# Performance work log

Hardware: AMD Instinct MI355X
Metric: run time of the kernel (lower is better)

The kernel has to match this reference:

```python
import jax, jax.numpy as jnp
import numpy as np

B = 1
DIM = 2048
N_HEADS = 16
HEAD_DIM = 128
RANK = 128
ALPHA = 128.0
L_NOISE = 2048
L_COND = 1024
N_LORAS = 1
EPS = 1e-6
NEG = -1e20


def setup_inputs() -> dict:
    key = jax.random.key(0)
    ks = jax.random.split(key, 24)
    inp = {}
    inp["noise_flat"] = jax.random.normal(ks[0], (B, L_NOISE, DIM), jnp.float32)
    inp["cond_flat"] = jax.random.normal(ks[1], (B, L_COND, DIM), jnp.float32)
    # RoPE freqs in TE 'bshd' convention: (L, head_dim), halves duplicated
    inv_freq = 1.0 / (10000.0 ** (jnp.arange(0, HEAD_DIM, 2, dtype=jnp.float32) / HEAD_DIM))
    pos = jnp.arange(L_NOISE + L_COND, dtype=jnp.float32)
    fr = pos[:, None] * inv_freq[None, :]
    fr = jnp.concatenate([fr, fr], axis=-1)  # (L, HEAD_DIM)
    inp["noise_rope"] = fr[:L_NOISE]
    inp["cond_rope"] = fr[L_NOISE:]
    std = 0.02
    inp["Wq"] = jax.random.normal(ks[2], (DIM, DIM), jnp.float32) * std
    inp["Wk"] = jax.random.normal(ks[3], (DIM, DIM), jnp.float32) * std
    inp["Wv"] = jax.random.normal(ks[4], (DIM, DIM), jnp.float32) * std
    inp["Wo"] = jax.random.normal(ks[5], (DIM, DIM), jnp.float32) * std
    inp["bq"] = jnp.zeros((DIM,), jnp.float32)
    inp["bk"] = jnp.zeros((DIM,), jnp.float32)
    inp["bv"] = jnp.zeros((DIM,), jnp.float32)
    inp["bo"] = jnp.zeros((DIM,), jnp.float32)
    inp["q_norm_scale"] = jnp.ones((HEAD_DIM,), jnp.float32)
    inp["k_norm_scale"] = jnp.ones((HEAD_DIM,), jnp.float32)
    inp["v_norm_scale"] = jnp.ones((HEAD_DIM,), jnp.float32)
    # LoRA: down ~ N(0, 1/rank); up small nonzero (torch inits zeros, made nonzero for a meaningful baseline)
    for name, ki in zip(["q", "k", "v", "o"], range(6, 10)):
        k1, k2 = jax.random.split(ks[ki])
        inp[f"lora_{name}_down"] = jax.random.normal(k1, (DIM, RANK), jnp.float32) / RANK
        inp[f"lora_{name}_up"] = jax.random.normal(k2, (RANK, DIM), jnp.float32) * 0.01
    return inp


def _rms_norm(x, scale):
    return x * jax.lax.rsqrt(jnp.mean(x * x, axis=-1, keepdims=True) + EPS) * scale


def _rotate_half(x):
    x1, x2 = jnp.split(x, 2, axis=-1)
    return jnp.concatenate([-x2, x1], axis=-1)


def _apply_rope(x, freqs):
    # x: (B, L, H, D), freqs: (L, D)
    cos = jnp.cos(freqs)[None, :, None, :]
    sin = jnp.sin(freqs)[None, :, None, :]
    return x * cos + _rotate_half(x) * sin


def _block_mask():
    # noise rows attend to everything; cond block i attends only to itself
    L = L_NOISE + L_COND * N_LORAS
    idx = jnp.arange(L)
    is_noise = idx < L_NOISE
    blk = (idx - L_NOISE) // L_COND
    allowed = is_noise[:, None] | (
        (~is_noise[:, None]) & (~is_noise[None, :]) & (blk[:, None] == blk[None, :])
    )
    return jnp.where(allowed, 0.0, NEG).astype(jnp.float32)  # (L, L)


def _cond_mask(i, L):
    idx = jnp.arange(L)
    start = L_NOISE + i * L_COND
    return ((idx >= start) & (idx < start + L_COND)).astype(jnp.float32)[None, :, None]


def reference(noise_flat, cond_flat, noise_rope, cond_rope,
              Wq, Wk, Wv, Wo, bq, bk, bv, bo,
              q_norm_scale, k_norm_scale, v_norm_scale,
              lora_q_down, lora_q_up, lora_k_down, lora_k_up,
              lora_v_down, lora_v_up, lora_o_down, lora_o_up):
    joint = jnp.concatenate([noise_flat, cond_flat], axis=1)  # (B, L, D)
    rope = jnp.concatenate([noise_rope, cond_rope], axis=0)   # (L, HEAD_DIM)
    L = joint.shape[1]
    scale_lora = ALPHA / RANK
    m = _cond_mask(0, L)  # n_loras = 1, lora_weight = 1.0
    jm = joint * m

    def lora(x_masked, Wd, Wu):
        return (x_masked @ Wd) @ Wu * scale_lora

    q = joint @ Wq + bq + lora(jm, lora_q_down, lora_q_up)
    k = joint @ Wk + bk + lora(jm, lora_k_down, lora_k_up)
    v = joint @ Wv + bv + lora(jm, lora_v_down, lora_v_up)

    q = q.reshape(B, L, N_HEADS, HEAD_DIM)
    k = k.reshape(B, L, N_HEADS, HEAD_DIM)
    v = v.reshape(B, L, N_HEADS, HEAD_DIM)
    q = _rms_norm(q, q_norm_scale)
    k = _rms_norm(k, k_norm_scale)
    v = _rms_norm(v, v_norm_scale)
    q = _apply_rope(q, rope)
    k = _apply_rope(k, rope)

    bias = _block_mask()[None, None]  # (1,1,L,L)
    scores = jnp.einsum('bqhd,bkhd->bhqk', q, k) / jnp.sqrt(jnp.float32(HEAD_DIM)) + bias
    attn = jax.nn.softmax(scores, axis=-1)
    x = jnp.einsum('bhqk,bkhd->bqhd', attn, v).reshape(B, L, DIM)

    out = x @ Wo + bo + lora(x * m, lora_o_down, lora_o_up)
    return out[:, :L_NOISE, :], out[:, L_NOISE:, :]
```

## Files before the change

kernel.cpp:

```cpp
#include <hip/hip_runtime.h>

typedef _Float16 f16;
typedef _Float16 half8 __attribute__((ext_vector_type(8)));
typedef float floatx4 __attribute__((ext_vector_type(4)));

#define L_TOT   3072
#define L_NZ    2048
#define DIM_C   2048
#define NH      16
#define HD      128

__device__ __forceinline__ void gl_lds16(const f16* g, f16* l) {
    __builtin_amdgcn_global_load_lds((__attribute__((address_space(1))) void*)g,
                                     (__attribute__((address_space(3))) void*)l,
                                     16, 0, 0);
}

__global__ void sentinel_kernel(float* out) { out[0] = 1.0e6f; }

__global__ __launch_bounds__(256)
void cast_joint(const float* __restrict__ noise, const float* __restrict__ cond,
                f16* __restrict__ out) {
    int i = (blockIdx.x * 256 + threadIdx.x) * 4;
    const float* src; int off;
    if (i < 2048 * 2048) { src = noise; off = i; }
    else                 { src = cond;  off = i - 2048 * 2048; }
    float4 v = *(const float4*)(src + off);
    out[i+0] = (f16)v.x; out[i+1] = (f16)v.y;
    out[i+2] = (f16)v.z; out[i+3] = (f16)v.w;
}

__global__ __launch_bounds__(256)
void transpose_cast4(const float* __restrict__ s0, const float* __restrict__ s1,
                     const float* __restrict__ s2, const float* __restrict__ s3,
                     f16* __restrict__ dstBase, int R, int C, long long outBatch) {
    const float* in = (blockIdx.z == 0) ? s0 : (blockIdx.z == 1) ? s1 : (blockIdx.z == 2) ? s2 : s3;
    f16* out = dstBase + (long long)blockIdx.z * outBatch;
    __shared__ f16 tile[32][33];
    int x = threadIdx.x & 31, y0 = threadIdx.x >> 5;
    int r0 = blockIdx.y * 32, c0 = blockIdx.x * 32;
#pragma unroll
    for (int i = 0; i < 4; ++i) {
        int y = y0 + i * 8;
        tile[y][x] = (f16)in[(size_t)(r0 + y) * C + (c0 + x)];
    }
    __syncthreads();
#pragma unroll
    for (int i = 0; i < 4; ++i) {
        int y = y0 + i * 8;
        out[(size_t)(c0 + y) * R + (r0 + x)] = tile[x][y];
    }
}

template<int WRITE_HALF, int ACCUM, int ADD_BIAS, int MODE>
__global__ __launch_bounds__(256, 2)
void gemm_tn(const f16* __restrict__ A, const f16* __restrict__ BT,
             void* __restrict__ Cv,
             const float* __restrict__ bias0, const float* __restrict__ bias1,
             const float* __restrict__ bias2,
             int M, int N, int K, int lda, int ldb, int ldc, float cscale) {
    __shared__ __align__(16) f16 lds[2][2][128 * 64];
    const int tid  = threadIdx.x;
    const int lane = tid & 63, wave = tid >> 6;
    const int m0 = blockIdx.y * 128, n0 = blockIdx.x * 128;
    const int wr = wave >> 1, wc = wave & 1;
    floatx4 acc[4][4] = {};

    if (MODE == 2) A += (size_t)(n0 >> 11) * 128;

    const int r0i = tid >> 3;
    const int gch = (tid & 7) ^ (r0i & 7);
    const f16* gA0 = A  + (size_t)(m0 + r0i) * lda + gch * 8;
    const f16* gB0 = BT + (size_t)(n0 + r0i) * ldb + gch * 8;
    const int ldsW = wave * 512;

    auto stage = [&](int buf, int k0) {
#pragma unroll
        for (int is = 0; is < 4; ++is)
            gl_lds16(gA0 + k0 + (size_t)is * 32 * lda, &lds[buf][0][0] + is * 2048 + ldsW);
#pragma unroll
        for (int is = 0; is < 4; ++is)
            gl_lds16(gB0 + k0 + (size_t)is * 32 * ldb, &lds[buf][1][0] + is * 2048 + ldsW);
    };

    const int rl = lane & 15, cq = lane >> 4;

    const int nIter = K >> 6;
    stage(0, 0);
    int cur = 0;
    for (int t = 0; t < nIter; ++t) {
        const int k0n = (t + 1 < nIter) ? (t + 1) * 64 : 0;
        stage(cur ^ 1, k0n);
        asm volatile("s_waitcnt vmcnt(8)" ::: "memory");
        __builtin_amdgcn_s_barrier();
        __builtin_amdgcn_sched_barrier(0);

#pragma unroll
        for (int kh = 0; kh < 2; ++kh) {
            half8 af[4], bf[4];
#pragma unroll
            for (int m = 0; m < 4; ++m) {
                int row = wr * 64 + m * 16 + rl;
                int pos = (kh * 4 + cq) ^ (row & 7);
                af[m] = *(const half8*)(&lds[cur][0][row * 64 + pos * 8]);
            }
#pragma unroll
            for (int n = 0; n < 4; ++n) {
                int row = wc * 64 + n * 16 + rl;
                int pos = (kh * 4 + cq) ^ (row & 7);
                bf[n] = *(const half8*)(&lds[cur][1][row * 64 + pos * 8]);
            }
#pragma unroll
            for (int m = 0; m < 4; ++m)
#pragma unroll
                for (int n = 0; n < 4; ++n)
                    acc[m][n] = __builtin_amdgcn_mfma_f32_16x16x32_f16(af[m], bf[n], acc[m][n], 0, 0, 0);
        }
        __builtin_amdgcn_s_barrier();
        __builtin_amdgcn_sched_barrier(0);
        cur ^= 1;
    }

    const int rq = lane >> 4;
    const float* bias = bias0;
    size_t cbase = 0;
    if (MODE == 1 || MODE == 2) {
        int chunk = n0 >> 11;
        if (MODE == 1) bias = (chunk == 0) ? bias0 : ((chunk == 1) ? bias1 : bias2);
        cbase = (size_t)chunk * ((size_t)L_TOT * DIM_C);
    }
#pragma unroll
    for (int m = 0; m < 4; ++m) {
        int row = m0 + wr * 64 + m * 16 + rq * 4;
#pragma unroll
        for (int n = 0; n < 4; ++n) {
            int col = n0 + wc * 64 + n * 16 + rl;
            int ccol = (MODE == 1 || MODE == 2) ? (col & 2047) : col;
            float badd = ADD_BIAS ? bias[ccol] : 0.0f;
#pragma unroll
            for (int j = 0; j < 4; ++j) {
                float v = acc[m][n][j] * cscale + badd;
                size_t idx = cbase + (size_t)(row + j) * ldc + ccol;
                if (WRITE_HALF) {
                    f16* C = (f16*)Cv;
                    if (ACCUM) v += (float)C[idx];
                    C[idx] = (f16)v;
                } else {
                    float* C = (float*)Cv;
                    if (ACCUM) v += C[idx];
                    C[idx] = v;
                }
            }
        }
    }
}

__global__ __launch_bounds__(256)
void norm_rope_v(const f16* __restrict__ q16, const f16* __restrict__ k16, const f16* __restrict__ v16,
                 const float* __restrict__ qs, const float* __restrict__ ks, const float* __restrict__ vs,
                 const float* __restrict__ nrope, const float* __restrict__ crope,
                 f16* __restrict__ qH, f16* __restrict__ kH, f16* __restrict__ vT) {
    __shared__ f16 vtile[128][33];
    const int t = threadIdx.x, rloc = t >> 3, c = t & 7;
    const int r = blockIdx.x * 32 + rloc, h = blockIdx.y;
    const int d0 = c * 8;
    const size_t src = (size_t)r * DIM_C + h * HD;
    half8 qlv = *(const half8*)(q16 + src + d0);
    half8 qhv = *(const half8*)(q16 + src + 64 + d0);
    half8 klv = *(const half8*)(k16 + src + d0);
    half8 khv = *(const half8*)(k16 + src + 64 + d0);
    half8 vlv = *(const half8*)(v16 + src + d0);
    half8 vhv = *(const half8*)(v16 + src + 64 + d0);
    float ql[8], qh[8], kl[8], kh[8], vl[8], vh[8];
    float sq = 0.f, sk = 0.f, sv = 0.f;
#pragma unroll
    for (int i = 0; i < 8; ++i) {
        ql[i] = (float)qlv[i]; qh[i] = (float)qhv[i];
        kl[i] = (float)klv[i]; kh[i] = (float)khv[i];
        vl[i] = (float)vlv[i]; vh[i] = (float)vhv[i];
        sq += ql[i]*ql[i] + qh[i]*qh[i];
        sk += kl[i]*kl[i] + kh[i]*kh[i];
        sv += vl[i]*vl[i] + vh[i]*vh[i];
    }
    sq += __shfl_xor(sq, 1); sq += __shfl_xor(sq, 2); sq += __shfl_xor(sq, 4);
    sk += __shfl_xor(sk, 1); sk += __shfl_xor(sk, 2); sk += __shfl_xor(sk, 4);
    sv += __shfl_xor(sv, 1); sv += __shfl_xor(sv, 2); sv += __shfl_xor(sv, 4);
    const float rqs = rsqrtf(sq * (1.0f / 128.0f) + 1e-6f);
    const float rks = rsqrtf(sk * (1.0f / 128.0f) + 1e-6f);
    const float rvs = rsqrtf(sv * (1.0f / 128.0f) + 1e-6f);
    const float* rp = (r < L_NZ) ? (nrope + (size_t)r * HD) : (crope + (size_t)(r - L_NZ) * HD);
    half8 qo_l, qo_h, ko_l, ko_h;
#pragma unroll
    for (int i = 0; i < 8; ++i) {
        float fr = rp[d0 + i];
        float cs = cosf(fr), sn = sinf(fr);
        float qnl = ql[i] * rqs * qs[d0 + i],      qnh = qh[i] * rqs * qs[64 + d0 + i];
        float knl = kl[i] * rks * ks[d0 + i],      knh = kh[i] * rks * ks[64 + d0 + i];
        qo_l[i] = (f16)((qnl * cs - qnh * sn) * 0.08838834764831845f);
        qo_h[i] = (f16)((qnh * cs + qnl * sn) * 0.08838834764831845f);
        ko_l[i] = (f16)(knl * cs - knh * sn);
        ko_h[i] = (f16)(knh * cs + knl * sn);
        vtile[d0 + i][rloc]      = (f16)(vl[i] * rvs * vs[d0 + i]);
        vtile[64 + d0 + i][rloc] = (f16)(vh[i] * rvs * vs[64 + d0 + i]);
    }
    const size_t dst = ((size_t)h * L_TOT + r) * HD;
    *(half8*)(qH + dst + d0) = qo_l;      *(half8*)(qH + dst + 64 + d0) = qo_h;
    *(half8*)(kH + dst + d0) = ko_l;      *(half8*)(kH + dst + 64 + d0) = ko_h;
    __syncthreads();
    const int dd = t >> 1, seg = (t & 1) * 16;
    half8 o0, o1;
#pragma unroll
    for (int i = 0; i < 8; ++i) { o0[i] = vtile[dd][seg + i]; o1[i] = vtile[dd][seg + 8 + i]; }
    f16* vdst = vT + ((size_t)h * HD + dd) * L_TOT + blockIdx.x * 32 + seg;
    *(half8*)(vdst)     = o0;
    *(half8*)(vdst + 8) = o1;
}

__global__ __launch_bounds__(256, 2)
void flash_kernel(const f16* __restrict__ qH, const f16* __restrict__ kH,
                  const f16* __restrict__ vT, f16* __restrict__ xH) {
    __shared__ __align__(16) f16 lds_k[2][64 * 128];
    __shared__ __align__(16) f16 lds_v[64 * 128];
    __shared__ __align__(16) f16 p_lds[4][32][72];
    const int tid = threadIdx.x;
    const int lane = tid & 63, w = tid >> 6;
    const int bid = blockIdx.x;
    const int xcd = bid & 7, rr = bid >> 3;
    int h, qb;
    if (rr < 16) { h = xcd + 8 * (rr >> 3); qb = 16 + (rr & 7); }
    else         { int li = rr - 16; h = xcd + 8 * (li >> 4); qb = li & 15; }
    const int q0 = qb * 128 + w * 32;
    const int rl = lane & 15, rq = lane >> 4;

    half8 aq[2][4];
    const f16* qbase = qH + ((size_t)h * L_TOT + q0) * HD;
#pragma unroll
    for (int qt = 0; qt < 2; ++qt)
#pragma unroll
        for (int kc = 0; kc < 4; ++kc)
            aq[qt][kc] = *(const half8*)(qbase + (size_t)(qt * 16 + rl) * HD + kc * 32 + rq * 8);

    floatx4 acc[2][8] = {};
    floatx4 accl[2] = {};
    const half8 vone = {(f16)1.f, (f16)1.f, (f16)1.f, (f16)1.f,
                        (f16)1.f, (f16)1.f, (f16)1.f, (f16)1.f};

    const int kLo = (qb >= 16) ? L_NZ : 0;
    const f16* khead = kH + (size_t)h * L_TOT * HD;
    const f16* vhead = vT + (size_t)h * HD * L_TOT;

    auto stageK = [&](int kb, int pb) {
#pragma unroll
        for (int is = 0; is < 4; ++is) {
            int i = is * 256 + tid;
            int r = i >> 4, c = i & 15;
            gl_lds16(khead + (size_t)(kb + r) * HD + ((c ^ (r & 15)) * 8),
                     &lds_k[pb][0] + (is * 256 + w * 64) * 8);
        }
    };
    auto stageV = [&](int kb) {
#pragma unroll
        for (int is = 0; is < 4; ++is) {
            int i = is * 256 + tid;
            int pair = i >> 4, c10 = i & 15;
            int g10 = c10 ^ (pair & 15);
            int d = pair * 2 + (g10 >> 3), kchunk = g10 & 7;
            gl_lds16(vhead + (size_t)d * L_TOT + kb + kchunk * 8,
                     lds_v + (is * 256 + w * 64) * 8);
        }
    };

    asm volatile("s_waitcnt vmcnt(0)" ::: "memory");
    stageK(kLo, 0);
    int p = 0;
    for (int kb = kLo; kb < L_TOT; kb += 64) {
        const int kbn = (kb + 64 < L_TOT) ? (kb + 64) : kLo;
        stageV(kb);
        stageK(kbn, p ^ 1);
        asm volatile("s_waitcnt vmcnt(8)" ::: "memory");
        __builtin_amdgcn_s_barrier();
        __builtin_amdgcn_sched_barrier(0);

        const f16* kbase = &lds_k[p][0];
        floatx4 sacc[2][4] = {};
        __builtin_amdgcn_s_setprio(1);
#pragma unroll
        for (int kf = 0; kf < 4; ++kf) {
            int r = kf * 16 + rl;
#pragma unroll
            for (int kc = 0; kc < 4; ++kc) {
                half8 bk = *(const half8*)(kbase + r * 128 + (((kc * 4 + rq) ^ (r & 15)) * 8));
                sacc[0][kf] = __builtin_amdgcn_mfma_f32_16x16x32_f16(aq[0][kc], bk, sacc[0][kf], 0, 0, 0);
                sacc[1][kf] = __builtin_amdgcn_mfma_f32_16x16x32_f16(aq[1][kc], bk, sacc[1][kf], 0, 0, 0);
            }
        }
        __builtin_amdgcn_s_setprio(0);
#pragma unroll
        for (int qt = 0; qt < 2; ++qt)
#pragma unroll
            for (int kf = 0; kf < 4; ++kf)
#pragma unroll
                for (int j = 0; j < 4; ++j) {
                    float pv = __expf(sacc[qt][kf][j] - 4.0f);
                    p_lds[w][qt * 16 + rq * 4 + j][kf * 16 + rl] = (f16)pv;
                }

        asm volatile("s_waitcnt vmcnt(4)" ::: "memory");
        __builtin_amdgcn_s_barrier();
        __builtin_amdgcn_sched_barrier(0);

        __builtin_amdgcn_s_setprio(1);
#pragma unroll
        for (int kc = 0; kc < 2; ++kc) {
            half8 ap0 = *(const half8*)(&p_lds[w][0 * 16 + rl][kc * 32 + rq * 8]);
            half8 ap1 = *(const half8*)(&p_lds[w][1 * 16 + rl][kc * 32 + rq * 8]);
            accl[0] = __builtin_amdgcn_mfma_f32_16x16x32_f16(ap0, vone, accl[0], 0, 0, 0);
            accl[1] = __builtin_amdgcn_mfma_f32_16x16x32_f16(ap1, vone, accl[1], 0, 0, 0);
#pragma unroll
            for (int dt = 0; dt < 8; ++dt) {
                int d = dt * 16 + rl;
                int g10 = (d & 1) * 8 + kc * 4 + rq;
                half8 bv = *(const half8*)(lds_v + (d >> 1) * 128 + ((g10 ^ ((d >> 1) & 15)) * 8));
                acc[0][dt] = __builtin_amdgcn_mfma_f32_16x16x32_f16(ap0, bv, acc[0][dt], 0, 0, 0);
                acc[1][dt] = __builtin_amdgcn_mfma_f32_16x16x32_f16(ap1, bv, acc[1][dt], 0, 0, 0);
            }
        }
        __builtin_amdgcn_s_setprio(0);
        __builtin_amdgcn_s_barrier();
        p ^= 1;
    }

#pragma unroll
    for (int qt = 0; qt < 2; ++qt)
#pragma unroll
        for (int j = 0; j < 4; ++j) {
            float li = 1.0f / accl[qt][j];
            int row = q0 + qt * 16 + rq * 4 + j;
#pragma unroll
            for (int dt = 0; dt < 8; ++dt)
                xH[(size_t)row * DIM_C + h * HD + dt * 16 + rl] = (f16)(acc[qt][dt][j] * li);
        }
}

extern "C" void kernel_launch(void* const* d_in, const int* in_sizes, int n_in,
                              void* d_out, int out_size, void* d_ws, size_t ws_size,
                              hipStream_t stream) {
    const float* noise = (const float*)d_in[0];
    const float* cond  = (const float*)d_in[1];
    const float* nrope = (const float*)d_in[2];
    const float* crope = (const float*)d_in[3];
    const float* Wq = (const float*)d_in[4];
    const float* Wk = (const float*)d_in[5];
    const float* Wv = (const float*)d_in[6];
    const float* Wo = (const float*)d_in[7];
    const float* bq = (const float*)d_in[8];
    const float* bk = (const float*)d_in[9];
    const float* bv = (const float*)d_in[10];
    const float* bo = (const float*)d_in[11];
    const float* qs = (const float*)d_in[12];
    const float* ks = (const float*)d_in[13];
    const float* vs = (const float*)d_in[14];
    const float* lqd = (const float*)d_in[15];
    const float* lqu = (const float*)d_in[16];
    const float* lkd = (const float*)d_in[17];
    const float* lku = (const float*)d_in[18];
    const float* lvd = (const float*)d_in[19];
    const float* lvu = (const float*)d_in[20];
    const float* lod = (const float*)d_in[21];
    const float* lou = (const float*)d_in[22];
    (void)in_sizes; (void)n_in; (void)out_size;

    char* ws = (char*)d_ws;
    const size_t SZ_LD = (size_t)L_TOT * DIM_C * sizeof(f16);
    const size_t SZ_W  = (size_t)DIM_C * DIM_C * sizeof(f16);
    size_t o = 0;
    auto take = [&](size_t b) { size_t r = o; o += (b + 255) & ~(size_t)255; return r; };
    f16* jointH = (f16*)(ws + take(SZ_LD));
    f16* WTqkv  = (f16*)(ws + take(4 * SZ_W));
    f16* WT3    = WTqkv + (size_t)3 * 2048 * 2048;
    f16* downT  = (f16*)(ws + take((size_t)4 * 128 * 2048 * 2));
    f16* downTo = downT + (size_t)3 * 128 * 2048;
    f16* upT    = (f16*)(ws + take((size_t)4 * 2048 * 128 * 2));
    f16* upTo   = upT + (size_t)3 * 2048 * 128;
    f16* q16    = (f16*)(ws + take(3 * SZ_LD));
    f16* k16    = q16 + (size_t)L_TOT * DIM_C;
    f16* v16    = k16 + (size_t)L_TOT * DIM_C;
    f16* t_all  = (f16*)(ws + take((size_t)1024 * 384 * 2));
    f16* t_o    = (f16*)(ws + take((size_t)1024 * 128 * 2));
    f16* qHd    = (f16*)(ws + take(SZ_LD));
    f16* kHd    = (f16*)(ws + take(SZ_LD));
    f16* vTd    = (f16*)(ws + take(SZ_LD));
    f16* xH     = (f16*)(ws + take(SZ_LD));
    if (o > ws_size) {
        sentinel_kernel<<<1, 1, 0, stream>>>((float*)d_out);
        return;
    }

    cast_joint<<<dim3(6144), 256, 0, stream>>>(noise, cond, jointH);
    transpose_cast4<<<dim3(64, 64, 4), 256, 0, stream>>>(Wq, Wk, Wv, Wo, WTqkv, 2048, 2048,
                                                         (long long)2048 * 2048);
    transpose_cast4<<<dim3(4, 64, 4), 256, 0, stream>>>(lqd, lkd, lvd, lod, downT, 2048, 128,
                                                        (long long)128 * 2048);
    transpose_cast4<<<dim3(64, 4, 4), 256, 0, stream>>>(lqu, lku, lvu, lou, upT, 128, 2048,
                                                        (long long)2048 * 128);

    gemm_tn<1, 0, 1, 1><<<dim3(48, 24), 256, 0, stream>>>(
        jointH, WTqkv, q16, bq, bk, bv, 3072, 6144, 2048, 2048, 2048, 2048, 1.0f);
    gemm_tn<1, 0, 0, 0><<<dim3(3, 8), 256, 0, stream>>>(jointH + (size_t)2048 * 2048, downT, t_all,
                                                        nullptr, nullptr, nullptr,
                                                        1024, 384, 2048, 2048, 2048, 384, 1.0f);
    gemm_tn<1, 1, 0, 2><<<dim3(48, 8), 256, 0, stream>>>(t_all, upT, q16 + (size_t)2048 * 2048,
                                                         nullptr, nullptr, nullptr,
                                                         1024, 6144, 128, 384, 128, 2048, 1.0f);

    norm_rope_v<<<dim3(96, 16), 256, 0, stream>>>(q16, k16, v16, qs, ks, vs, nrope, crope,
                                                  qHd, kHd, vTd);

    flash_kernel<<<dim3(384), 256, 0, stream>>>(qHd, kHd, vTd, xH);

    gemm_tn<0, 0, 1, 0><<<dim3(16, 24), 256, 0, stream>>>(xH, WT3, d_out, bo, nullptr, nullptr,
                                                          3072, 2048, 2048, 2048, 2048, 2048, 1.0f);
    gemm_tn<1, 0, 0, 0><<<dim3(1, 8), 256, 0, stream>>>(xH + (size_t)2048 * 2048, downTo, t_o,
                                                        nullptr, nullptr, nullptr,
                                                        1024, 128, 2048, 2048, 2048, 128, 1.0f);
    gemm_tn<0, 1, 0, 0><<<dim3(16, 8), 256, 0, stream>>>(t_o, upTo, (float*)d_out + (size_t)2048 * 2048,
                                                         nullptr, nullptr, nullptr,
                                                         1024, 2048, 128, 128, 128, 2048, 1.0f);
}
```

Before: 355.6 us.

## Merge independent GEMMs into paired launches and halve flash attention query tile

Adds a gemm_pair kernel that runs two independent GEMMs in one grid: the QKV projection with the LoRA down-projection, and the output projection with the output LoRA down-projection. This removes the serialized small launches and their tail underutilization. Flash attention now gives each wave 16 query rows instead of 32, doubling the block count to 768 for better CU occupancy and load balance, but each K/V tile loaded into LDS is reused across fewer query rows. The gemm_tn template is simplified by dropping the unused cscale and extra bias arguments.

```diff
diff --git a/kernel.cpp b/kernel.cpp
--- a/kernel.cpp
+++ b/kernel.cpp
@@ -56,9 +56,8 @@
 __global__ __launch_bounds__(256, 2)
 void gemm_tn(const f16* __restrict__ A, const f16* __restrict__ BT,
              void* __restrict__ Cv,
-             const float* __restrict__ bias0, const float* __restrict__ bias1,
-             const float* __restrict__ bias2,
-             int M, int N, int K, int lda, int ldb, int ldc, float cscale) {
+             const float* __restrict__ bias0,
+             int M, int N, int K, int lda, int ldb, int ldc) {
     __shared__ __align__(16) f16 lds[2][2][128 * 64];
     const int tid  = threadIdx.x;
     const int lane = tid & 63, wave = tid >> 6;
@@ -94,7 +93,6 @@
         asm volatile("s_waitcnt vmcnt(8)" ::: "memory");
         __builtin_amdgcn_s_barrier();
         __builtin_amdgcn_sched_barrier(0);
-
 #pragma unroll
         for (int kh = 0; kh < 2; ++kh) {
             half8 af[4], bf[4];
@@ -122,24 +120,19 @@
     }
 
     const int rq = lane >> 4;
-    const float* bias = bias0;
     size_t cbase = 0;
-    if (MODE == 1 || MODE == 2) {
-        int chunk = n0 >> 11;
-        if (MODE == 1) bias = (chunk == 0) ? bias0 : ((chunk == 1) ? bias1 : bias2);
-        cbase = (size_t)chunk * ((size_t)L_TOT * DIM_C);
-    }
+    if (MODE == 2) cbase = (size_t)(n0 >> 11) * ((size_t)L_TOT * DIM_C);
 #pragma unroll
     for (int m = 0; m < 4; ++m) {
         int row = m0 + wr * 64 + m * 16 + rq * 4;
 #pragma unroll
         for (int n = 0; n < 4; ++n) {
             int col = n0 + wc * 64 + n * 16 + rl;
-            int ccol = (MODE == 1 || MODE == 2) ? (col & 2047) : col;
-            float badd = ADD_BIAS ? bias[ccol] : 0.0f;
+            int ccol = (MODE == 2) ? (col & 2047) : col;
+            float badd = ADD_BIAS ? bias0[ccol] : 0.0f;
 #pragma unroll
             for (int j = 0; j < 4; ++j) {
-                float v = acc[m][n][j] * cscale + badd;
+                float v = acc[m][n][j] + badd;
                 size_t idx = cbase + (size_t)(row + j) * ldc + ccol;
                 if (WRITE_HALF) {
                     f16* C = (f16*)Cv;
@@ -150,6 +143,112 @@
                     if (ACCUM) v += C[idx];
                     C[idx] = v;
                 }
+            }
+        }
+    }
+}
+
+__global__ __launch_bounds__(256, 2)
+void gemm_pair(int nb0, int nbx0,
+               const f16* __restrict__ A0, const f16* __restrict__ BT0, void* C0,
+               const float* __restrict__ b00, const float* __restrict__ b01, const float* __restrict__ b02,
+               int lda0, int ldb0, int ldc0, int wh0, int ab0, int mode0,
+               int nbx1,
+               const f16* __restrict__ A1, const f16* __restrict__ BT1, void* C1,
+               int lda1, int ldb1, int ldc1, int wh1,
+               int K) {
+    __shared__ __align__(16) f16 lds[2][2][128 * 64];
+    const int tid  = threadIdx.x;
+    const int lane = tid & 63, wave = tid >> 6;
+    const int bid = blockIdx.x;
+    const bool j0 = (bid < nb0);
+    const int lb  = j0 ? bid : (bid - nb0);
+    const int nbx = j0 ? nbx0 : nbx1;
+    const int bx = lb % nbx, by = lb / nbx;
+    const int m0 = by * 128, n0 = bx * 128;
+    const f16* A  = j0 ? A0  : A1;
+    const f16* BT = j0 ? BT0 : BT1;
+    const int lda = j0 ? lda0 : lda1, ldb = j0 ? ldb0 : ldb1, ldc = j0 ? ldc0 : ldc1;
+    const int wr = wave >> 1, wc = wave & 1;
+    floatx4 acc[4][4] = {};
+
+    const int r0i = tid >> 3;
+    const int gch = (tid & 7) ^ (r0i & 7);
+    const f16* gA0 = A  + (size_t)(m0 + r0i) * lda + gch * 8;
+    const f16* gB0 = BT + (size_t)(n0 + r0i) * ldb + gch * 8;
+    const int ldsW = wave * 512;
+
+    auto stage = [&](int buf, int k0) {
+#pragma unroll
+        for (int is = 0; is < 4; ++is)
+            gl_lds16(gA0 + k0 + (size_t)is * 32 * lda, &lds[buf][0][0] + is * 2048 + ldsW);
+#pragma unroll
+        for (int is = 0; is < 4; ++is)
+            gl_lds16(gB0 + k0 + (size_t)is * 32 * ldb, &lds[buf][1][0] + is * 2048 + ldsW);
+    };
+
+    const int rl = lane & 15, cq = lane >> 4;
+    const int nIter = K >> 6;
+    stage(0, 0);
+    int cur = 0;
+    for (int t = 0; t < nIter; ++t) {
+        const int k0n = (t + 1 < nIter) ? (t + 1) * 64 : 0;
+        stage(cur ^ 1, k0n);
+        asm volatile("s_waitcnt vmcnt(8)" ::: "memory");
+        __builtin_amdgcn_s_barrier();
+        __builtin_amdgcn_sched_barrier(0);
+#pragma unroll
+        for (int kh = 0; kh < 2; ++kh) {
+            half8 af[4], bf[4];
+#pragma unroll
+            for (int m = 0; m < 4; ++m) {
+                int row = wr * 64 + m * 16 + rl;
+                int pos = (kh * 4 + cq) ^ (row & 7);
+                af[m] = *(const half8*)(&lds[cur][0][row * 64 + pos * 8]);
+            }
+#pragma unroll
+            for (int n = 0; n < 4; ++n) {
+                int row = wc * 64 + n * 16 + rl;
+                int pos = (kh * 4 + cq) ^ (row & 7);
+                bf[n] = *(const half8*)(&lds[cur][1][row * 64 + pos * 8]);
+            }
+#pragma unroll
+            for (int m = 0; m < 4; ++m)
+#pragma unroll
+                for (int n = 0; n < 4; ++n)
+                    acc[m][n] = __builtin_amdgcn_mfma_f32_16x16x32_f16(af[m], bf[n], acc[m][n], 0, 0, 0);
+        }
+        __builtin_amdgcn_s_barrier();
+        __builtin_amdgcn_sched_barrier(0);
+        cur ^= 1;
+    }
+
+    const int rq = lane >> 4;
+    const int wh = j0 ? wh0 : wh1;
+    const int ab = j0 ? ab0 : 0;
+    const int md = j0 ? mode0 : 0;
+    void* Cv = j0 ? C0 : C1;
+    size_t cbase = 0;
+    const float* bias = b00;
+    if (md == 1) {
+        int chunk = n0 >> 11;
+        bias = (chunk == 0) ? b00 : ((chunk == 1) ? b01 : b02);
+        cbase = (size_t)chunk * ((size_t)L_TOT * DIM_C);
+    }
+#pragma unroll
+    for (int m = 0; m < 4; ++m) {
+        int row = m0 + wr * 64 + m * 16 + rq * 4;
+#pragma unroll
+        for (int n = 0; n < 4; ++n) {
+            int col = n0 + wc * 64 + n * 16 + rl;
+            int ccol = (md == 1) ? (col & 2047) : col;
+            float badd = ab ? bias[ccol] : 0.0f;
+#pragma unroll
+            for (int j = 0; j < 4; ++j) {
+                float v = acc[m][n][j] + badd;
+                size_t idx = cbase + (size_t)(row + j) * ldc + ccol;
+                if (wh) ((f16*)Cv)[idx] = (f16)v;
+                else    ((float*)Cv)[idx] = v;
             }
         }
     }
@@ -221,31 +320,29 @@
                   const f16* __restrict__ vT, f16* __restrict__ xH) {
     __shared__ __align__(16) f16 lds_k[2][64 * 128];
     __shared__ __align__(16) f16 lds_v[64 * 128];
-    __shared__ __align__(16) f16 p_lds[4][32][72];
+    __shared__ __align__(16) f16 p_lds[4][16][72];
     const int tid = threadIdx.x;
     const int lane = tid & 63, w = tid >> 6;
     const int bid = blockIdx.x;
     const int xcd = bid & 7, rr = bid >> 3;
     int h, qb;
-    if (rr < 16) { h = xcd + 8 * (rr >> 3); qb = 16 + (rr & 7); }
-    else         { int li = rr - 16; h = xcd + 8 * (li >> 4); qb = li & 15; }
-    const int q0 = qb * 128 + w * 32;
+    if (rr < 32) { h = xcd + 8 * (rr >> 4); qb = 32 + (rr & 15); }
+    else         { int li = rr - 32; h = xcd + 8 * (li >> 5); qb = li & 31; }
+    const int q0 = qb * 64 + w * 16;
     const int rl = lane & 15, rq = lane >> 4;
 
-    half8 aq[2][4];
+    half8 aq[4];
     const f16* qbase = qH + ((size_t)h * L_TOT + q0) * HD;
 #pragma unroll
-    for (int qt = 0; qt < 2; ++qt)
-#pragma unroll
-        for (int kc = 0; kc < 4; ++kc)
-            aq[qt][kc] = *(const half8*)(qbase + (size_t)(qt * 16 + rl) * HD + kc * 32 + rq * 8);
-
-    floatx4 acc[2][8] = {};
-    floatx4 accl[2] = {};
+    for (int kc = 0; kc < 4; ++kc)
+        aq[kc] = *(const half8*)(qbase + (size_t)rl * HD + kc * 32 + rq * 8);
+
+    floatx4 acc[8] = {};
+    floatx4 accl = {};
     const half8 vone = {(f16)1.f, (f16)1.f, (f16)1.f, (f16)1.f,
                         (f16)1.f, (f16)1.f, (f16)1.f, (f16)1.f};
 
-    const int kLo = (qb >= 16) ? L_NZ : 0;
+    const int kLo = (qb >= 32) ? L_NZ : 0;
     const f16* khead = kH + (size_t)h * L_TOT * HD;
     const f16* vhead = vT + (size_t)h * HD * L_TOT;
 
@@ -282,7 +379,7 @@
         __builtin_amdgcn_sched_barrier(0);
 
         const f16* kbase = &lds_k[p][0];
-        floatx4 sacc[2][4] = {};
+        floatx4 sacc[4] = {};
         __builtin_amdgcn_s_setprio(1);
 #pragma unroll
         for (int kf = 0; kf < 4; ++kf) {
@@ -290,20 +387,17 @@
 #pragma unroll
             for (int kc = 0; kc < 4; ++kc) {
                 half8 bk = *(const half8*)(kbase + r * 128 + (((kc * 4 + rq) ^ (r & 15)) * 8));
-                sacc[0][kf] = __builtin_amdgcn_mfma_f32_16x16x32_f16(aq[0][kc], bk, sacc[0][kf], 0, 0, 0);
-                sacc[1][kf] = __builtin_amdgcn_mfma_f32_16x16x32_f16(aq[1][kc], bk, sacc[1][kf], 0, 0, 0);
+                sacc[kf] = __builtin_amdgcn_mfma_f32_16x16x32_f16(aq[kc], bk, sacc[kf], 0, 0, 0);
             }
         }
         __builtin_amdgcn_s_setprio(0);
 #pragma unroll
-        for (int qt = 0; qt < 2; ++qt)
-#pragma unroll
-            for (int kf = 0; kf < 4; ++kf)
-#pragma unroll
-                for (int j = 0; j < 4; ++j) {
-                    float pv = __expf(sacc[qt][kf][j] - 4.0f);
-                    p_lds[w][qt * 16 + rq * 4 + j][kf * 16 + rl] = (f16)pv;
-                }
+        for (int kf = 0; kf < 4; ++kf)
+#pragma unroll
+            for (int j = 0; j < 4; ++j) {
+                float pv = __expf(sacc[kf][j] - 4.0f);
+                p_lds[w][rq * 4 + j][kf * 16 + rl] = (f16)pv;
+            }
 
         asm volatile("s_waitcnt vmcnt(4)" ::: "memory");
         __builtin_amdgcn_s_barrier();
@@ -312,17 +406,14 @@
         __builtin_amdgcn_s_setprio(1);
 #pragma unroll
         for (int kc = 0; kc < 2; ++kc) {
-            half8 ap0 = *(const half8*)(&p_lds[w][0 * 16 + rl][kc * 32 + rq * 8]);
-            half8 ap1 = *(const half8*)(&p_lds[w][1 * 16 + rl][kc * 32 + rq * 8]);
-            accl[0] = __builtin_amdgcn_mfma_f32_16x16x32_f16(ap0, vone, accl[0], 0, 0, 0);
-            accl[1] = __builtin_amdgcn_mfma_f32_16x16x32_f16(ap1, vone, accl[1], 0, 0, 0);
+            half8 ap = *(const half8*)(&p_lds[w][rl][kc * 32 + rq * 8]);
+            accl = __builtin_amdgcn_mfma_f32_16x16x32_f16(ap, vone, accl, 0, 0, 0);
 #pragma unroll
             for (int dt = 0; dt < 8; ++dt) {
                 int d = dt * 16 + rl;
                 int g10 = (d & 1) * 8 + kc * 4 + rq;
                 half8 bv = *(const half8*)(lds_v + (d >> 1) * 128 + ((g10 ^ ((d >> 1) & 15)) * 8));
-                acc[0][dt] = __builtin_amdgcn_mfma_f32_16x16x32_f16(ap0, bv, acc[0][dt], 0, 0, 0);
-                acc[1][dt] = __builtin_amdgcn_mfma_f32_16x16x32_f16(ap1, bv, acc[1][dt], 0, 0, 0);
+                acc[dt] = __builtin_amdgcn_mfma_f32_16x16x32_f16(ap, bv, acc[dt], 0, 0, 0);
             }
         }
         __builtin_amdgcn_s_setprio(0);
@@ -331,15 +422,13 @@
     }
 
 #pragma unroll
-    for (int qt = 0; qt < 2; ++qt)
-#pragma unroll
-        for (int j = 0; j < 4; ++j) {
-            float li = 1.0f / accl[qt][j];
-            int row = q0 + qt * 16 + rq * 4 + j;
-#pragma unroll
-            for (int dt = 0; dt < 8; ++dt)
-                xH[(size_t)row * DIM_C + h * HD + dt * 16 + rl] = (f16)(acc[qt][dt][j] * li);
-        }
+    for (int j = 0; j < 4; ++j) {
+        float li = 1.0f / accl[j];
+        int row = q0 + rq * 4 + j;
+#pragma unroll
+        for (int dt = 0; dt < 8; ++dt)
+            xH[(size_t)row * DIM_C + h * HD + dt * 16 + rl] = (f16)(acc[dt][j] * li);
+    }
 }
 
 extern "C" void kernel_launch(void* const* d_in, const int* in_sizes, int n_in,
@@ -404,26 +493,22 @@
     transpose_cast4<<<dim3(64, 4, 4), 256, 0, stream>>>(lqu, lku, lvu, lou, upT, 128, 2048,
                                                         (long long)2048 * 128);
 
-    gemm_tn<1, 0, 1, 1><<<dim3(48, 24), 256, 0, stream>>>(
-        jointH, WTqkv, q16, bq, bk, bv, 3072, 6144, 2048, 2048, 2048, 2048, 1.0f);
-    gemm_tn<1, 0, 0, 0><<<dim3(3, 8), 256, 0, stream>>>(jointH + (size_t)2048 * 2048, downT, t_all,
-                                                        nullptr, nullptr, nullptr,
-                                                        1024, 384, 2048, 2048, 2048, 384, 1.0f);
+    gemm_pair<<<dim3(1152 + 24), 256, 0, stream>>>(
+        1152, 48, jointH, WTqkv, q16, bq, bk, bv, 2048, 2048, 2048, 1, 1, 1,
+        3, jointH + (size_t)2048 * 2048, downT, t_all, 2048, 2048, 384, 1,
+        2048);
     gemm_tn<1, 1, 0, 2><<<dim3(48, 8), 256, 0, stream>>>(t_all, upT, q16 + (size_t)2048 * 2048,
-                                                         nullptr, nullptr, nullptr,
-                                                         1024, 6144, 128, 384, 128, 2048, 1.0f);
+                                                         nullptr, 1024, 6144, 128, 384, 128, 2048);
 
     norm_rope_v<<<dim3(96, 16), 256, 0, stream>>>(q16, k16, v16, qs, ks, vs, nrope, crope,
                                                   qHd, kHd, vTd);
 
-    flash_kernel<<<dim3(384), 256, 0, stream>>>(qHd, kHd, vTd, xH);
-
-    gemm_tn<0, 0, 1, 0><<<dim3(16, 24), 256, 0, stream>>>(xH, WT3, d_out, bo, nullptr, nullptr,
-                                                          3072, 2048, 2048, 2048, 2048, 2048, 1.0f);
-    gemm_tn<1, 0, 0, 0><<<dim3(1, 8), 256, 0, stream>>>(xH + (size_t)2048 * 2048, downTo, t_o,
-                                                        nullptr, nullptr, nullptr,
-                                                        1024, 128, 2048, 2048, 2048, 128, 1.0f);
+    flash_kernel<<<dim3(768), 256, 0, stream>>>(qHd, kHd, vTd, xH);
+
+    gemm_pair<<<dim3(384 + 8), 256, 0, stream>>>(
+        384, 16, xH, WT3, d_out, bo, nullptr, nullptr, 2048, 2048, 2048, 0, 1, 0,
+        1, xH + (size_t)2048 * 2048, downTo, t_o, 2048, 2048, 128, 1,
+        2048);
     gemm_tn<0, 1, 0, 0><<<dim3(16, 8), 256, 0, stream>>>(t_o, upTo, (float*)d_out + (size_t)2048 * 2048,
-                                                         nullptr, nullptr, nullptr,
-                                                         1024, 2048, 128, 128, 128, 2048, 1.0f);
-}
+                                                         nullptr, 1024, 2048, 128, 128, 128, 2048);
+}
```

New measurement: 338.4 us. -4.8%, faster.
